# Optimization experiments

Measured on AMD Instinct MI355X. Metric: run time of the kernel, lower is better.

The kernel has to match this reference:

```python
import jax, jax.numpy as jnp
import numpy as np

NUM_BINS_X = 128; NUM_BINS_Y = 128
XL, XH, YL, YH = 0.0, 1000.0, 0.0, 1000.0
NUM_NETS = 100000
NUM_NODES = 200000
NUM_MOVABLE = 180000
NUM_PINS = 400000
UNIT_H_CAP = 1.5
UNIT_V_CAP = 1.4
MAX_RATE = 2.0
MIN_RATE = 1.0 / MAX_RATE
BIN_SX = (XH - XL) / NUM_BINS_X
BIN_SY = (YH - YL) / NUM_BINS_Y


def setup_inputs() -> dict:
    key = jax.random.key(0)
    k1, k2, k3, k4, k5, k6, k7, k8 = jax.random.split(key, 8)
    pos = jnp.concatenate([
        jax.random.uniform(k1, (NUM_NODES,), jnp.float32, XL, XH - 8.0),
        jax.random.uniform(k2, (NUM_NODES,), jnp.float32, YL, YH - 8.0)])
    pin_pos = jnp.concatenate([
        jax.random.uniform(k3, (NUM_PINS,), jnp.float32, XL, XH),
        jax.random.uniform(k4, (NUM_PINS,), jnp.float32, YL, YH)])
    node_size_x = jax.random.uniform(k5, (NUM_NODES,), jnp.float32, 1.0, 8.0)
    node_size_y = jax.random.uniform(k6, (NUM_NODES,), jnp.float32, 1.0, 8.0)
    # 4 pins per net (uniform ragged layout); flat_netpin is a permutation of pins
    netpin_start = jnp.arange(NUM_NETS + 1, dtype=jnp.int32) * (NUM_PINS // NUM_NETS)
    flat_netpin = jax.random.permutation(k7, NUM_PINS).astype(jnp.int32)
    net_weights = jax.random.uniform(k8, (NUM_NETS,), jnp.float32, 0.5, 1.5)
    return dict(pos=pos, pin_pos=pin_pos, node_size_x=node_size_x,
                node_size_y=node_size_y, net_weights=net_weights,
                netpin_start=netpin_start, flat_netpin=flat_netpin)


def _bin_edges(lo, size, n):
    l = lo + jnp.arange(n, dtype=jnp.float32) * size
    return l, l + size


def _overlap(lo_e, hi_e, lo, hi):
    # per-interval overlap of [lo, hi] with each bin [lo_e, hi_e]; >=0
    return jnp.clip(jnp.minimum(hi_e[None, :], hi[:, None]) -
                    jnp.maximum(lo_e[None, :], lo[:, None]), 0.0, None)


def reference(pos, pin_pos, node_size_x, node_size_y, net_weights,
              netpin_start, flat_netpin):
    # ---- phase 1: per-net bbox (ragged gather) + RUDY demand binning ----
    lengths = netpin_start[1:] - netpin_start[:-1]                      # [N]
    net_ids = jnp.repeat(jnp.arange(NUM_NETS, dtype=jnp.int32), lengths,
                         total_repeat_length=NUM_PINS)                  # [P]
    px = pin_pos[flat_netpin]
    py = pin_pos[flat_netpin + NUM_PINS]
    x_min = jax.ops.segment_min(px, net_ids, num_segments=NUM_NETS)
    x_max = jax.ops.segment_max(px, net_ids, num_segments=NUM_NETS)
    y_min = jax.ops.segment_min(py, net_ids, num_segments=NUM_NETS)
    y_max = jax.ops.segment_max(py, net_ids, num_segments=NUM_NETS)

    bxl, bxr = _bin_edges(XL, BIN_SX, NUM_BINS_X)
    byl, byr = _bin_edges(YL, BIN_SY, NUM_BINS_Y)
    ox = _overlap(bxl, bxr, x_min, x_max)                               # [N, BX]
    oy = _overlap(byl, byr, y_min, y_max)                               # [N, BY]
    dx = x_max - x_min
    dy = y_max - y_min
    # horizontal demand per bin = wt * overlap / (y_max - y_min); vertical analog
    cx = jnp.where(dy > 0, net_weights / jnp.where(dy > 0, dy, 1.0), 0.0)
    cy = jnp.where(dx > 0, net_weights / jnp.where(dx > 0, dx, 1.0), 0.0)
    map_x = jnp.einsum('nx,ny->xy', ox * cx[:, None], oy)               # [BX, BY]
    map_y = jnp.einsum('nx,ny->xy', ox * cy[:, None], oy)

    bin_area = BIN_SX * BIN_SY
    ux = map_x / (bin_area * UNIT_H_CAP)
    uy = map_y / (bin_area * UNIT_V_CAP)
    util = jnp.clip(jnp.maximum(ux, uy), MIN_RATE, MAX_RATE)            # [BX, BY]

    # ---- phase 2: per movable node, overlap-weighted utilization read-back ----
    nx = pos[:NUM_MOVABLE]
    ny = pos[NUM_NODES:NUM_NODES + NUM_MOVABLE]
    sx = node_size_x[:NUM_MOVABLE]
    sy = node_size_y[:NUM_MOVABLE]
    oxn = _overlap(bxl, bxr, nx, nx + sx)                               # [M, BX]
    oyn = _overlap(byl, byr, ny, ny + sy)                               # [M, BY]
    tmp = jnp.einsum('mx,xy->my', oxn, util)                            # [M, BY]
    instance_route_area = jnp.sum(tmp * oyn, axis=1)                    # [M]
    return instance_route_area
```

## Files before the change

kernel.cpp:

```cpp
#include <hip/hip_runtime.h>

constexpr int   NB         = 128;
constexpr int   NCELL      = NB * NB;
constexpr int   NFL        = 2 * NCELL;
constexpr float S          = 7.8125f;
constexpr int   NUM_NETS   = 100000;
constexpr int   NUM_NODES  = 200000;
constexpr int   NUM_MOVABLE= 180000;
constexpr int   NUM_PINS   = 400000;
constexpr float UNIT_H_CAP = 1.5f;
constexpr float UNIT_V_CAP = 1.4f;

#define TPB    1024
#define NDB    128
#define NCHUNK 8

__device__ __forceinline__ float edgef(int t) { return (float)t * S; }

__device__ __forceinline__ int bin_of(float v) {
    int t = (int)floorf(v / S);
    while (edgef(t + 1) <= v) ++t;
    while (edgef(t)     >  v) --t;
    return t;
}

__device__ __forceinline__ float phi(int t, float lo, float hi) {
    return fminf(fmaxf(edgef(t), lo), hi);
}

__device__ __forceinline__ int second_diff(float lo, float hi,
                                           int* idx, float* val) {
    int a = bin_of(lo);
    int b = bin_of(hi);
    int n = 0;
    idx[n] = a;
    val[n] = phi(a + 1, lo, hi) - 2.f * phi(a, lo, hi) + phi(a - 1, lo, hi);
    ++n;
    idx[n] = a + 1;
    val[n] = phi(a + 2, lo, hi) - 2.f * phi(a + 1, lo, hi) + phi(a, lo, hi);
    ++n;
    if (b > a + 1) {
        idx[n] = b;
        val[n] = phi(b + 1, lo, hi) - 2.f * phi(b, lo, hi) + phi(b - 1, lo, hi);
        ++n;
    }
    if (b > a) {
        idx[n] = b + 1;
        val[n] = phi(b + 2, lo, hi) - 2.f * phi(b + 1, lo, hi) + phi(b, lo, hi);
        ++n;
    }
    return n;
}

__global__ __launch_bounds__(TPB) void net_diff_kernel(
    const float* __restrict__ pin_pos,
    const float* __restrict__ net_weights,
    const int*   __restrict__ nps,
    const int*   __restrict__ fnp,
    float* __restrict__ P) {
    extern __shared__ float Dl[];
    const int tid = threadIdx.x;

    float4* D4 = (float4*)Dl;
    for (int i = tid; i < NFL / 4; i += TPB) D4[i] = make_float4(0, 0, 0, 0);
    __syncthreads();

    const int per = (NUM_NETS + gridDim.x - 1) / gridDim.x;
    const int n0  = blockIdx.x * per;
    const int n1  = min(n0 + per, NUM_NETS);

    for (int n = n0 + tid; n < n1; n += TPB) {
        int s = nps[n], e = nps[n + 1];
        if (e <= s) continue;
        float xmin, xmax, ymin, ymax;
        if (e - s == 4 && (s & 3) == 0) {
            int4 p4 = *(const int4*)(fnp + s);
            float x0 = pin_pos[p4.x], y0 = pin_pos[p4.x + NUM_PINS];
            float x1 = pin_pos[p4.y], y1 = pin_pos[p4.y + NUM_PINS];
            float x2 = pin_pos[p4.z], y2 = pin_pos[p4.z + NUM_PINS];
            float x3 = pin_pos[p4.w], y3 = pin_pos[p4.w + NUM_PINS];
            xmin = fminf(fminf(x0, x1), fminf(x2, x3));
            xmax = fmaxf(fmaxf(x0, x1), fmaxf(x2, x3));
            ymin = fminf(fminf(y0, y1), fminf(y2, y3));
            ymax = fmaxf(fmaxf(y0, y1), fmaxf(y2, y3));
        } else {
            xmin = 1e30f; xmax = -1e30f; ymin = 1e30f; ymax = -1e30f;
            for (int p = s; p < e; ++p) {
                int pin = fnp[p];
                float px = pin_pos[pin];
                float py = pin_pos[pin + NUM_PINS];
                xmin = fminf(xmin, px); xmax = fmaxf(xmax, px);
                ymin = fminf(ymin, py); ymax = fmaxf(ymax, py);
            }
        }
        float w  = net_weights[n];
        float dx = xmax - xmin, dy = ymax - ymin;
        float cx = (dy > 0.f) ? w / dy : 0.f;
        float cy = (dx > 0.f) ? w / dx : 0.f;
        if (cx == 0.f && cy == 0.f) continue;

        int ixs[4], iys[4];
        float vxs[4], vys[4];
        int nx = second_diff(xmin, xmax, ixs, vxs);
        int ny = second_diff(ymin, ymax, iys, vys);

        for (int i = 0; i < nx; ++i) {
            int row = ixs[i];
            float fi = vxs[i];
            if (fi == 0.f || row >= NB) continue;
            for (int j = 0; j < ny; ++j) {
                int col = iys[j];
                float t = fi * vys[j];
                if (t == 0.f || col >= NB) continue;
                int cell = row * NB + col;
                if (cx != 0.f) atomicAdd(&Dl[cell],         cx * t);
                if (cy != 0.f) atomicAdd(&Dl[NCELL + cell], cy * t);
            }
        }
    }
    __syncthreads();

    float4* Pb = (float4*)(P + (size_t)blockIdx.x * NFL);
    for (int i = tid; i < NFL / 4; i += TPB) Pb[i] = D4[i];
}

__global__ __launch_bounds__(256) void reduce_kernel(
    const float4* __restrict__ P,
    float4* __restrict__ Rc,
    int B) {
    constexpr int NF4 = NFL / 4;
    int g = blockIdx.x * blockDim.x + threadIdx.x;
    int chunk = blockIdx.y;
    int per = (B + NCHUNK - 1) / NCHUNK;
    int b0 = chunk * per;
    int b1 = min(b0 + per, B);
    float4 a0 = {0,0,0,0}, a1 = {0,0,0,0}, a2 = {0,0,0,0}, a3 = {0,0,0,0};
    int b = b0;
    for (; b + 3 < b1; b += 4) {
        float4 v0 = P[(size_t)(b    ) * NF4 + g];
        float4 v1 = P[(size_t)(b + 1) * NF4 + g];
        float4 v2 = P[(size_t)(b + 2) * NF4 + g];
        float4 v3 = P[(size_t)(b + 3) * NF4 + g];
        a0.x += v0.x; a0.y += v0.y; a0.z += v0.z; a0.w += v0.w;
        a1.x += v1.x; a1.y += v1.y; a1.z += v1.z; a1.w += v1.w;
        a2.x += v2.x; a2.y += v2.y; a2.z += v2.z; a2.w += v2.w;
        a3.x += v3.x; a3.y += v3.y; a3.z += v3.z; a3.w += v3.w;
    }
    for (; b < b1; ++b) {
        float4 v = P[(size_t)b * NF4 + g];
        a0.x += v.x; a0.y += v.y; a0.z += v.z; a0.w += v.w;
    }
    float4 r;
    r.x = (a0.x + a1.x) + (a2.x + a3.x);
    r.y = (a0.y + a1.y) + (a2.y + a3.y);
    r.z = (a0.z + a1.z) + (a2.z + a3.z);
    r.w = (a0.w + a1.w) + (a2.w + a3.w);
    Rc[(size_t)chunk * NF4 + g] = r;
}

__global__ __launch_bounds__(NB) void scan_x_kernel(
    const float* __restrict__ Rc,
    float2* __restrict__ Xp) {
    __shared__ float2 sm[NB];
    int col = blockIdx.x;
    int t = threadIdx.x;
    int idx = t * NB + col;
    float2 v = make_float2(0.f, 0.f);
    #pragma unroll
    for (int c = 0; c < NCHUNK; ++c) {
        v.x += Rc[(size_t)c * NFL + idx];
        v.y += Rc[(size_t)c * NFL + NCELL + idx];
    }
    sm[t] = v;
    __syncthreads();
    #pragma unroll
    for (int off = 1; off < NB; off <<= 1) {
        float2 cur = sm[t];
        float2 add = (t >= off) ? sm[t - off] : make_float2(0.f, 0.f);
        __syncthreads();
        cur.x += add.x; cur.y += add.y;
        sm[t] = cur;
        __syncthreads();
    }
    Xp[idx] = sm[t];
}

__global__ __launch_bounds__(NB) void scan_y_kernel(
    const float2* __restrict__ Xp,
    float* __restrict__ util) {
    __shared__ float2 sm[NB];
    int row = blockIdx.x;
    int t = threadIdx.x;
    sm[t] = Xp[row * NB + t];
    __syncthreads();
    #pragma unroll
    for (int off = 1; off < NB; off <<= 1) {
        float2 cur = sm[t];
        float2 add = (t >= off) ? sm[t - off] : make_float2(0.f, 0.f);
        __syncthreads();
        cur.x += add.x; cur.y += add.y;
        sm[t] = cur;
        __syncthreads();
    }
    constexpr float invx = 1.f / (S * S * UNIT_H_CAP);
    constexpr float invy = 1.f / (S * S * UNIT_V_CAP);
    float2 r = sm[t];
    float u = fmaxf(r.x * invx, r.y * invy);
    util[row * NB + t] = fminf(fmaxf(u, 0.5f), 2.0f);
}

__global__ __launch_bounds__(256) void node_kernel(
    const float* __restrict__ pos,
    const float* __restrict__ nsx,
    const float* __restrict__ nsy,
    const float* __restrict__ util,
    float* __restrict__ out) {
    int m = blockIdx.x * blockDim.x + threadIdx.x;
    if (m >= NUM_MOVABLE) return;
    float x  = pos[m];
    float y  = pos[NUM_NODES + m];
    float xh = x + nsx[m];
    float yh = y + nsy[m];
    int ax = max(0,      (int)floorf(x  / S) - 1);
    int bx = min(NB - 1, (int)floorf(xh / S) + 1);
    int ay = max(0,      (int)floorf(y  / S) - 1);
    int by = min(NB - 1, (int)floorf(yh / S) + 1);
    float acc = 0.f;
    for (int i = ax; i <= bx; ++i) {
        float ov = fminf(edgef(i + 1), xh) - fmaxf(edgef(i), x);
        if (ov <= 0.f) continue;
        float inner = 0.f;
        for (int j = ay; j <= by; ++j) {
            float ovy = fminf(edgef(j + 1), yh) - fmaxf(edgef(j), y);
            if (ovy > 0.f) inner += ovy * util[i * NB + j];
        }
        acc += ov * inner;
    }
    out[m] = acc;
}

extern "C" void kernel_launch(void* const* d_in, const int* in_sizes, int n_in,
                              void* d_out, int out_size, void* d_ws, size_t ws_size,
                              hipStream_t stream) {
    const float* pos      = (const float*)d_in[0];
    const float* pin_pos  = (const float*)d_in[1];
    const float* nsx      = (const float*)d_in[2];
    const float* nsy      = (const float*)d_in[3];
    const float* nw       = (const float*)d_in[4];
    const int*   npstart  = (const int*)d_in[5];
    const int*   fnp      = (const int*)d_in[6];
    float*       out      = (float*)d_out;

    float* w    = (float*)d_ws;
    float* Rc   = w;                           w += NCHUNK * NFL;
    float* Xp   = w;                           w += NFL;
    float* util = w;                           w += NCELL;
    float* P    = w;

    size_t fixed = (size_t)(w - (float*)d_ws) * sizeof(float);
    int B = NDB;
    if (ws_size > fixed) {
        size_t fit = (ws_size - fixed) / ((size_t)NFL * sizeof(float));
        if ((size_t)B > fit) B = (int)fit;
    } else {
        B = 1;
    }
    if (B < 1) B = 1;

    (void)hipFuncSetAttribute((const void*)net_diff_kernel,
                              hipFuncAttributeMaxDynamicSharedMemorySize,
                              NFL * (int)sizeof(float));

    net_diff_kernel<<<B, TPB, NFL * sizeof(float), stream>>>(
        pin_pos, nw, npstart, fnp, P);
    {
        dim3 g(NFL / 4 / 256, NCHUNK);
        reduce_kernel<<<g, 256, 0, stream>>>(
            (const float4*)P, (float4*)Rc, B);
    }
    scan_x_kernel<<<NB, NB, 0, stream>>>(Rc, (float2*)Xp);
    scan_y_kernel<<<NB, NB, 0, stream>>>((const float2*)Xp, util);
    node_kernel<<<(NUM_MOVABLE + 255) / 256, 256, 0, stream>>>(
        pos, nsx, nsy, util, out);
}
```

Measured before the change: 127.1 us.

## Split net bbox computation into separate high-occupancy kernel before LDS scatter

Result: slower. 135.9 us (+6.9%).

```diff
diff --git a/kernel.cpp b/kernel.cpp
--- a/kernel.cpp
+++ b/kernel.cpp
@@ -52,11 +52,53 @@
     return n;
 }
 
-__global__ __launch_bounds__(TPB) void net_diff_kernel(
+__global__ __launch_bounds__(256) void bbox_kernel(
     const float* __restrict__ pin_pos,
     const float* __restrict__ net_weights,
     const int*   __restrict__ nps,
     const int*   __restrict__ fnp,
+    float4* __restrict__ bbox,
+    float2* __restrict__ cxy) {
+    int n = blockIdx.x * 256 + threadIdx.x;
+    if (n >= NUM_NETS) return;
+    int s = nps[n], e = nps[n + 1];
+    if (e <= s) {
+        bbox[n] = make_float4(0.f, 0.f, 0.f, 0.f);
+        cxy[n]  = make_float2(0.f, 0.f);
+        return;
+    }
+    float xmin, xmax, ymin, ymax;
+    if (e - s == 4 && (s & 3) == 0) {
+        int4 p4 = *(const int4*)(fnp + s);
+        float x0 = pin_pos[p4.x], y0 = pin_pos[p4.x + NUM_PINS];
+        float x1 = pin_pos[p4.y], y1 = pin_pos[p4.y + NUM_PINS];
+        float x2 = pin_pos[p4.z], y2 = pin_pos[p4.z + NUM_PINS];
+        float x3 = pin_pos[p4.w], y3 = pin_pos[p4.w + NUM_PINS];
+        xmin = fminf(fminf(x0, x1), fminf(x2, x3));
+        xmax = fmaxf(fmaxf(x0, x1), fmaxf(x2, x3));
+        ymin = fminf(fminf(y0, y1), fminf(y2, y3));
+        ymax = fmaxf(fmaxf(y0, y1), fmaxf(y2, y3));
+    } else {
+        xmin = 1e30f; xmax = -1e30f; ymin = 1e30f; ymax = -1e30f;
+        for (int p = s; p < e; ++p) {
+            int pin = fnp[p];
+            float px = pin_pos[pin];
+            float py = pin_pos[pin + NUM_PINS];
+            xmin = fminf(xmin, px); xmax = fmaxf(xmax, px);
+            ymin = fminf(ymin, py); ymax = fmaxf(ymax, py);
+        }
+    }
+    float w  = net_weights[n];
+    float dx = xmax - xmin, dy = ymax - ymin;
+    float cx = (dy > 0.f) ? w / dy : 0.f;
+    float cy = (dx > 0.f) ? w / dx : 0.f;
+    bbox[n] = make_float4(xmin, xmax, ymin, ymax);
+    cxy[n]  = make_float2(cx, cy);
+}
+
+__global__ __launch_bounds__(TPB) void scatter_kernel(
+    const float4* __restrict__ bbox,
+    const float2* __restrict__ cxy,
     float* __restrict__ P) {
     extern __shared__ float Dl[];
     const int tid = threadIdx.x;
@@ -70,39 +112,15 @@
     const int n1  = min(n0 + per, NUM_NETS);
 
     for (int n = n0 + tid; n < n1; n += TPB) {
-        int s = nps[n], e = nps[n + 1];
-        if (e <= s) continue;
-        float xmin, xmax, ymin, ymax;
-        if (e - s == 4 && (s & 3) == 0) {
-            int4 p4 = *(const int4*)(fnp + s);
-            float x0 = pin_pos[p4.x], y0 = pin_pos[p4.x + NUM_PINS];
-            float x1 = pin_pos[p4.y], y1 = pin_pos[p4.y + NUM_PINS];
-            float x2 = pin_pos[p4.z], y2 = pin_pos[p4.z + NUM_PINS];
-            float x3 = pin_pos[p4.w], y3 = pin_pos[p4.w + NUM_PINS];
-            xmin = fminf(fminf(x0, x1), fminf(x2, x3));
-            xmax = fmaxf(fmaxf(x0, x1), fmaxf(x2, x3));
-            ymin = fminf(fminf(y0, y1), fminf(y2, y3));
-            ymax = fmaxf(fmaxf(y0, y1), fmaxf(y2, y3));
-        } else {
-            xmin = 1e30f; xmax = -1e30f; ymin = 1e30f; ymax = -1e30f;
-            for (int p = s; p < e; ++p) {
-                int pin = fnp[p];
-                float px = pin_pos[pin];
-                float py = pin_pos[pin + NUM_PINS];
-                xmin = fminf(xmin, px); xmax = fmaxf(xmax, px);
-                ymin = fminf(ymin, py); ymax = fmaxf(ymax, py);
-            }
-        }
-        float w  = net_weights[n];
-        float dx = xmax - xmin, dy = ymax - ymin;
-        float cx = (dy > 0.f) ? w / dy : 0.f;
-        float cy = (dx > 0.f) ? w / dx : 0.f;
+        float2 c = cxy[n];
+        float cx = c.x, cy = c.y;
         if (cx == 0.f && cy == 0.f) continue;
+        float4 bb = bbox[n];
 
         int ixs[4], iys[4];
         float vxs[4], vys[4];
-        int nx = second_diff(xmin, xmax, ixs, vxs);
-        int ny = second_diff(ymin, ymax, iys, vys);
+        int nx = second_diff(bb.x, bb.y, ixs, vxs);
+        int ny = second_diff(bb.z, bb.w, iys, vys);
 
         for (int i = 0; i < nx; ++i) {
             int row = ixs[i];
@@ -255,6 +273,8 @@
     float* Rc   = w;                           w += NCHUNK * NFL;
     float* Xp   = w;                           w += NFL;
     float* util = w;                           w += NCELL;
+    float* bbox = w;                           w += 4 * NUM_NETS;
+    float* cxy  = w;                           w += 2 * NUM_NETS;
     float* P    = w;
 
     size_t fixed = (size_t)(w - (float*)d_ws) * sizeof(float);
@@ -267,12 +287,14 @@
     }
     if (B < 1) B = 1;
 
-    (void)hipFuncSetAttribute((const void*)net_diff_kernel,
+    (void)hipFuncSetAttribute((const void*)scatter_kernel,
                               hipFuncAttributeMaxDynamicSharedMemorySize,
                               NFL * (int)sizeof(float));
 
-    net_diff_kernel<<<B, TPB, NFL * sizeof(float), stream>>>(
-        pin_pos, nw, npstart, fnp, P);
+    bbox_kernel<<<(NUM_NETS + 255) / 256, 256, 0, stream>>>(
+        pin_pos, nw, npstart, fnp, (float4*)bbox, (float2*)cxy);
+    scatter_kernel<<<B, TPB, NFL * sizeof(float), stream>>>(
+        (const float4*)bbox, (const float2*)cxy, P);
     {
         dim3 g(NFL / 4 / 256, NCHUNK);
         reduce_kernel<<<g, 256, 0, stream>>>(
```
